# Performance work log

Hardware: AMD Instinct MI355X
Metric: run time of the kernel (lower is better)

The kernel has to match this reference:

```python
import jax, jax.numpy as jnp
import numpy as np

N_NODES = 400
HID = 96
DEC = 64
FEAT_STATIC = 8
FEAT = FEAT_STATIC + N_NODES  # 408
EPS = 1e-8


def prelu(x, a):
    # single-parameter PReLU (torch default num_parameters=1)
    return jnp.where(x >= 0, x, a * x)


def setup_inputs() -> dict:
    key = jax.random.key(0)
    ks = jax.random.split(key, 16)
    B = 16
    E = N_NODES * (N_NODES - 1) // 2  # 79800

    x = jax.random.normal(ks[0], (B, E), dtype=jnp.float32)
    node_features = jax.random.normal(ks[1], (B, N_NODES, FEAT_STATIC), dtype=jnp.float32)
    sc_matrix = jax.random.uniform(ks[2], (B, N_NODES, N_NODES), dtype=jnp.float32)

    # normalization buffers (computed from train split in torch; random stand-ins)
    static_mean = jax.random.normal(ks[3], (1, 1, FEAT_STATIC), dtype=jnp.float32) * 0.1
    static_std = jnp.ones((1, 1, FEAT_STATIC), dtype=jnp.float32)

    def lin(k, fin, fout):
        kw, kb = jax.random.split(k)
        lim = 1.0 / np.sqrt(fin)
        W = jax.random.uniform(kw, (fin, fout), minval=-lim, maxval=lim, dtype=jnp.float32)
        b = jax.random.uniform(kb, (fout,), minval=-lim, maxval=lim, dtype=jnp.float32)
        return W, b

    W_e1, b_e1 = lin(ks[4], FEAT, HID)
    W_e2, b_e2 = lin(ks[5], HID, HID)
    W_d1, b_d1 = lin(ks[6], 3 * HID, DEC)  # symmetric decoder: 3 * node_embed_dim
    W_d2, b_d2 = lin(ks[7], DEC, DEC)
    W_d3, b_d3 = lin(ks[8], DEC, 1)

    a25 = jnp.float32(0.25)

    ei_np, ej_np = np.triu_indices(N_NODES, k=1)
    ei = jnp.asarray(ei_np, dtype=jnp.int32)
    ej = jnp.asarray(ej_np, dtype=jnp.int32)

    return {
        "x": x, "node_features": node_features, "sc_matrix": sc_matrix,
        "static_mean": static_mean, "static_std": static_std,
        "W_e1": W_e1, "b_e1": b_e1, "a_e1": a25,
        "W_e2": W_e2, "b_e2": b_e2, "a_e2": a25,
        "W_d1": W_d1, "b_d1": b_d1, "a_d1": a25,
        "W_d2": W_d2, "b_d2": b_d2, "a_d2": a25,
        "W_d3": W_d3, "b_d3": b_d3,
        "ei": ei, "ej": ej,
    }


def reference(x, node_features, sc_matrix, static_mean, static_std,
              W_e1, b_e1, a_e1, W_e2, b_e2, a_e2,
              W_d1, b_d1, a_d1, W_d2, b_d2, a_d2, W_d3, b_d3, ei, ej):
    # x (SC upper triangle) is only used for batch size in the torch module.
    # static anatomical block: z-score with train stats
    s = (node_features - static_mean) / (static_std + EPS)  # [B,N,8]
    # sc_row block, 'brain_scale': divide by per-matrix mean
    m = sc_matrix / jnp.maximum(
        jnp.mean(sc_matrix, axis=(-2, -1), keepdims=True), EPS)  # [B,N,N]
    feats = jnp.concatenate([s, m], axis=-1)  # [B,N,408]

    # shared node encoder (dropout inactive at eval)
    h = prelu(feats @ W_e1 + b_e1, a_e1)
    h = prelu(h @ W_e2 + b_e2, a_e2)  # [B,N,96]

    # per-edge gather over upper-triangle indices
    h_i = h[:, ei, :]  # [B,E,96]
    h_j = h[:, ej, :]
    # symmetric edge features
    edge_feat = jnp.concatenate(
        [h_i + h_j, jnp.abs(h_i - h_j), h_i * h_j], axis=-1)  # [B,E,288]

    z = prelu(edge_feat @ W_d1 + b_d1, a_d1)
    z = prelu(z @ W_d2 + b_d2, a_d2)
    out = (z @ W_d3 + b_d3)[..., 0]  # [B,E]
    return out
```

## Files before the change

kernel.cpp:

```cpp
#include <hip/hip_runtime.h>

#define NN 400
#define HID 96
#define EDGES 79800
#define BATCH 16
#define ROWS (BATCH*EDGES)
#define NTILES 4988
#define NBLK 512

typedef _Float16 f16;
typedef f16 f16x2 __attribute__((ext_vector_type(2)));
typedef f16 f16x8 __attribute__((ext_vector_type(8)));
typedef __fp16 fp16x2 __attribute__((ext_vector_type(2)));
typedef float f32x16 __attribute__((ext_vector_type(16)));
typedef unsigned int u32;

union H8 { f16x8 h; u32 u[4]; f16x2 p[4]; fp16x2 q[4]; };
union C2 { f16x2 h; fp16x2 q; u32 u; };

__device__ inline f16x2 pkrtz(float a, float b) {
  C2 c; c.q = __builtin_amdgcn_cvt_pkrtz(a, b); return c.h;
}
__device__ inline u32 pkrtz_u(float a, float b) {
  C2 c; c.q = __builtin_amdgcn_cvt_pkrtz(a, b); return c.u;
}
__device__ inline float fdot2a(f16x2 a, f16x2 b, float c) {
#if __has_builtin(__builtin_amdgcn_fdot2)
  C2 ca, cb; ca.h = a; cb.h = b;
  return __builtin_amdgcn_fdot2(ca.q, cb.q, c, false);
#else
  return c + (float)a.x*(float)b.x + (float)a.y*(float)b.y;
#endif
}

__device__ inline f16x8 habs8(f16x8 x) {
  H8 t; t.h = x;
  t.u[0] &= 0x7fff7fffu; t.u[1] &= 0x7fff7fffu;
  t.u[2] &= 0x7fff7fffu; t.u[3] &= 0x7fff7fffu;
  return t.h;
}

__device__ inline f16x8 pack8(float a0,float a1,float a2,float a3,
                              float a4,float a5,float a6,float a7){
  H8 u;
  u.p[0] = pkrtz(a0,a1);
  u.p[1] = pkrtz(a2,a3);
  u.p[2] = pkrtz(a4,a5);
  u.p[3] = pkrtz(a6,a7);
  return u.h;
}

__global__ void prep_mean_kernel(const float* __restrict__ We1, const float* __restrict__ We2,
                                 const float* __restrict__ W1, const float* __restrict__ W2,
                                 const float* __restrict__ sc,
                                 u32* __restrict__ wq, float* __restrict__ mpart) {
  if (blockIdx.x >= 140) {
    int p = blockIdx.x - 140;
    int b = p >> 2, part = p & 3;
    const float4* src = (const float4*)(sc + (size_t)b*160000) + part*10000;
    float s = 0.f;
    for (int i = threadIdx.x; i < 10000; i += 256) {
      float4 v = src[i];
      s += (v.x + v.y) + (v.z + v.w);
    }
    __shared__ float red[256];
    red[threadIdx.x] = s; __syncthreads();
    for (int off = 128; off > 0; off >>= 1) {
      if (threadIdx.x < off) red[threadIdx.x] += red[threadIdx.x + off];
      __syncthreads();
    }
    if (threadIdx.x == 0) mpart[p] = red[0];
    return;
  }
  int D = blockIdx.x*256 + threadIdx.x;
  float v0, v1;
  if (D < 9216) {
    int frag = D >> 8;  int t = frag >> 1, q = frag & 1;
    int rem = D & 255;  int lane = rem >> 2, dj = rem & 3;
    int c = lane & 31, h2 = lane >> 5;
    int k = 16*t + 8*h2 + 2*dj;
    int d = 32*q + c;
    v0 = W1[k*64 + d]; v1 = W1[(k+1)*64 + d];
  } else if (D < 11264) {
    int Dl = D - 9216;
    int frag = Dl >> 8; int t2 = frag >> 1, q = frag & 1;
    int rem = Dl & 255; int lane = rem >> 2, dj = rem & 3;
    int c = lane & 31, h2 = lane >> 5;
    int p = 8*t2 + 4*h2 + dj;
    int d = 32*q + c;
    v0 = W2[p*64 + d]; v1 = W2[(p+32)*64 + d];
  } else if (D < 31232) {
    int Dl = D - 11264;
    int frag = Dl >> 8; int t = frag/3, ct = frag - 3*t;
    int rem = Dl & 255; int lane = rem >> 2, dj = rem & 3;
    int c = lane & 31, h2 = lane >> 5;
    int k0 = 16*t + 8*h2 + 2*dj, k1 = k0 + 1;
    int d = 32*ct + c;
    v0 = (k0 < 400) ? We1[(8+k0)*96 + d] : (k0 < 408 ? We1[(k0-400)*96 + d] : 0.f);
    v1 = (k1 < 400) ? We1[(8+k1)*96 + d] : (k1 < 408 ? We1[(k1-400)*96 + d] : 0.f);
  } else {
    int Dl = D - 31232;
    int frag = Dl >> 8; int t = frag/3, ct = frag - 3*t;
    int rem = Dl & 255; int lane = rem >> 2, dj = rem & 3;
    int c = lane & 31, h2 = lane >> 5;
    int k = 16*t + 8*h2 + 2*dj;
    int d = 32*ct + c;
    v0 = We2[k*96 + d]; v1 = We2[(k+1)*96 + d];
  }
  wq[D] = pkrtz_u(v0, v1);
}

__global__ __launch_bounds__(64) void enc1_kernel(
    const float* __restrict__ sc, const float* __restrict__ nf,
    const float* __restrict__ smean, const float* __restrict__ sstd,
    const float* __restrict__ be1, const float* __restrict__ ae1,
    const float* __restrict__ mpart, const u32* __restrict__ wq,
    f16* __restrict__ g1) {
  int lane = threadIdx.x;
  int rt = blockIdx.x;
  int c = lane & 31, h2 = lane >> 5;
  int r = rt*32 + c;
  int b = r / 400;
  float ms = mpart[4*b] + mpart[4*b+1] + mpart[4*b+2] + mpart[4*b+3];
  float rm = 1.f / fmaxf(ms*(1.f/160000.f), 1e-8f);
  float a = *ae1;
  f32x16 acc[3];
#pragma unroll
  for (int q = 0; q < 3; ++q) {
    float bv = be1[32*q + c];
#pragma unroll
    for (int i = 0; i < 16; ++i) acc[q][i] = bv;
  }
  const u32* wb = wq + 11264;
  const float* scr = sc + (size_t)r*400;
#pragma unroll 4
  for (int t = 0; t < 25; ++t) {
    int k0 = 16*t + 8*h2;
    float4 s0 = *(const float4*)(scr + k0);
    float4 s1 = *(const float4*)(scr + k0 + 4);
    f16x8 af = pack8(s0.x*rm, s0.y*rm, s0.z*rm, s0.w*rm,
                     s1.x*rm, s1.y*rm, s1.z*rm, s1.w*rm);
#pragma unroll
    for (int ct = 0; ct < 3; ++ct) {
      f16x8 bf = *(const f16x8*)(wb + ((t*3+ct)*64 + lane)*4);
      acc[ct] = __builtin_amdgcn_mfma_f32_32x32x16_f16(af, bf, acc[ct], 0,0,0);
    }
  }
  {
    f16x8 af = {};
    if (h2 == 0) {
      float q0[8];
#pragma unroll
      for (int j = 0; j < 8; ++j)
        q0[j] = (nf[r*8 + j] - smean[j]) / (sstd[j] + 1e-8f);
      af = pack8(q0[0],q0[1],q0[2],q0[3],q0[4],q0[5],q0[6],q0[7]);
    }
#pragma unroll
    for (int ct = 0; ct < 3; ++ct) {
      f16x8 bf = *(const f16x8*)(wb + ((25*3+ct)*64 + lane)*4);
      acc[ct] = __builtin_amdgcn_mfma_f32_32x32x16_f16(af, bf, acc[ct], 0,0,0);
    }
  }
#pragma unroll
  for (int ct = 0; ct < 3; ++ct)
#pragma unroll
    for (int rr = 0; rr < 16; ++rr) {
      int row = (rr & 3) + 8*(rr >> 2) + 4*h2;
      float v = acc[ct][rr]; v = fmaxf(v, a*v);
      g1[(rt*32 + row)*96 + 32*ct + c] = (f16)v;
    }
}

__global__ __launch_bounds__(64) void enc2_kernel(
    const f16* __restrict__ g1, const float* __restrict__ be2,
    const float* __restrict__ ae2, const u32* __restrict__ wq,
    f16* __restrict__ hout) {
  int lane = threadIdx.x;
  int rt = blockIdx.x;
  int c = lane & 31, h2 = lane >> 5;
  int r = rt*32 + c;
  float a = *ae2;
  f32x16 acc[3];
#pragma unroll
  for (int q = 0; q < 3; ++q) {
    float bv = be2[32*q + c];
#pragma unroll
    for (int i = 0; i < 16; ++i) acc[q][i] = bv;
  }
  const u32* wb = wq + 31232;
#pragma unroll
  for (int t = 0; t < 6; ++t) {
    f16x8 af = *(const f16x8*)(g1 + r*96 + 16*t + 8*h2);
#pragma unroll
    for (int ct = 0; ct < 3; ++ct) {
      f16x8 bf = *(const f16x8*)(wb + ((t*3+ct)*64 + lane)*4);
      acc[ct] = __builtin_amdgcn_mfma_f32_32x32x16_f16(af, bf, acc[ct], 0,0,0);
    }
  }
#pragma unroll
  for (int ct = 0; ct < 3; ++ct)
#pragma unroll
    for (int rr = 0; rr < 16; ++rr) {
      int row = (rr & 3) + 8*(rr >> 2) + 4*h2;
      float v = acc[ct][rr]; v = fmaxf(v, a*v);
      hout[(rt*32 + row)*96 + 32*ct + c] = (f16)v;
    }
}

__global__ __launch_bounds__(256, 2) void decoder_kernel(
    const f16* __restrict__ hbuf, const u32* __restrict__ wq,
    const float* __restrict__ b1, const float* __restrict__ b2,
    const float* __restrict__ ad1, const float* __restrict__ ad2,
    const float* __restrict__ W3, const float* __restrict__ b3p,
    const int* __restrict__ ei, const int* __restrict__ ej,
    float* __restrict__ out) {
  __shared__ f16 wfr[17408];
  __shared__ u32 zbuf[4][1152];
  {
    float4* dst = (float4*)wfr;
    const float4* src = (const float4*)wq;
    for (int i = threadIdx.x; i < 2176; i += 256) dst[i] = src[i];
  }
  __syncthreads();
  const int lane = threadIdx.x & 63;
  const int wid  = threadIdx.x >> 6;
  const int c = lane & 31, h2 = lane >> 5;
  u32* zb = zbuf[wid];
  f16x8 bp5[2];
  bp5[0] = *(const f16x8*)(wq + ((34+0)*64 + lane)*4);
  bp5[1] = *(const f16x8*)(wq + ((34+1)*64 + lane)*4);
  f16x8 w2f[4][2];
#pragma unroll
  for (int t2 = 0; t2 < 4; ++t2) {
    w2f[t2][0] = *(const f16x8*)(wq + 9216 + ((t2*2+0)*64 + lane)*4);
    w2f[t2][1] = *(const f16x8*)(wq + 9216 + ((t2*2+1)*64 + lane)*4);
  }
  const float b1x = b1[c], b1y = b1[c+32];
  const float b2x = b2[c], b2y = b2[c+32];
  const float a1 = *ad1, a2 = *ad2, b3 = *b3p;
  const f16x2 a1v = pkrtz(a1, a1);
  const f16x2 a2v = pkrtz(a2, a2);
  const f16x2 w3p = pkrtz(W3[c], W3[c+32]);
  const f16x2 ones2 = pkrtz(1.f, 1.f);

  for (int tile = blockIdx.x; tile < NTILES; tile += NBLK) {
    const int rbase = tile*256 + wid*64;
    const f16* pi[2]; const f16* pj[2];
    bool valid[2];
#pragma unroll
    for (int m = 0; m < 2; ++m) {
      int r = rbase + 32*m + c;
      valid[m] = (r < ROWS);
      unsigned rr = valid[m] ? (unsigned)r : (unsigned)(ROWS-1);
      unsigned bb = rr / (unsigned)EDGES;
      int e = (int)(rr - bb*(unsigned)EDGES);
      int ii = ei[e], jj = ej[e];
      pi[m] = hbuf + (((int)bb*NN + ii)*HID + 8*h2);
      pj[m] = hbuf + (((int)bb*NN + jj)*HID + 8*h2);
    }
    f32x16 acc[2][2];
#pragma unroll
    for (int r = 0; r < 16; ++r) {
      acc[0][0][r] = b1x; acc[0][1][r] = b1y;
      acc[1][0][r] = b1x; acc[1][1][r] = b1y;
    }
#pragma unroll
    for (int t = 0; t < 6; ++t) {
      f16x8 bs0 = *(const f16x8*)(wfr + (((t   )*2+0)*64 + lane)*8);
      f16x8 bs1 = *(const f16x8*)(wfr + (((t   )*2+1)*64 + lane)*8);
      f16x8 bd0 = *(const f16x8*)(wfr + (((t+ 6)*2+0)*64 + lane)*8);
      f16x8 bd1 = *(const f16x8*)(wfr + (((t+ 6)*2+1)*64 + lane)*8);
      f16x8 bp0 = (t < 5) ? *(const f16x8*)(wfr + (((t+12)*2+0)*64 + lane)*8) : bp5[0];
      f16x8 bp1 = (t < 5) ? *(const f16x8*)(wfr + (((t+12)*2+1)*64 + lane)*8) : bp5[1];
#pragma unroll
      for (int m = 0; m < 2; ++m) {
        f16x8 hi = *(const f16x8*)(pi[m] + 16*t);
        f16x8 hj = *(const f16x8*)(pj[m] + 16*t);
        f16x8 su = hi + hj;
        f16x8 di = habs8(hi - hj);
        f16x8 pr = hi * hj;
        acc[m][0] = __builtin_amdgcn_mfma_f32_32x32x16_f16(su, bs0, acc[m][0], 0,0,0);
        acc[m][1] = __builtin_amdgcn_mfma_f32_32x32x16_f16(su, bs1, acc[m][1], 0,0,0);
        acc[m][0] = __builtin_amdgcn_mfma_f32_32x32x16_f16(di, bd0, acc[m][0], 0,0,0);
        acc[m][1] = __builtin_amdgcn_mfma_f32_32x32x16_f16(di, bd1, acc[m][1], 0,0,0);
        acc[m][0] = __builtin_amdgcn_mfma_f32_32x32x16_f16(pr, bp0, acc[m][0], 0,0,0);
        acc[m][1] = __builtin_amdgcn_mfma_f32_32x32x16_f16(pr, bp1, acc[m][1], 0,0,0);
      }
    }
#pragma unroll
    for (int m = 0; m < 2; ++m) {
#pragma unroll
      for (int r = 0; r < 16; ++r) {
        f16x2 p = pkrtz(acc[m][0][r], acc[m][1][r]);
        p = __builtin_elementwise_max(p, p * a1v);
        C2 cv; cv.h = p;
        int row = (r & 3) + 8*(r >> 2) + 4*h2;
        zb[row*36 + c] = cv.u;
      }
      f16x8 za[4];
#pragma unroll
      for (int t2 = 0; t2 < 4; ++t2)
        za[t2] = *(const f16x8*)((const f16*)zb + (c*36 + 8*t2 + 4*h2)*2);
      f32x16 zacc[2];
#pragma unroll
      for (int r = 0; r < 16; ++r) { zacc[0][r] = b2x; zacc[1][r] = b2y; }
#pragma unroll
      for (int t2 = 0; t2 < 4; ++t2) {
        zacc[0] = __builtin_amdgcn_mfma_f32_32x32x16_f16(za[t2], w2f[t2][0], zacc[0], 0,0,0);
        zacc[1] = __builtin_amdgcn_mfma_f32_32x32x16_f16(za[t2], w2f[t2][1], zacc[1], 0,0,0);
      }
#pragma unroll
      for (int r = 0; r < 16; ++r) {
        f16x2 p = pkrtz(zacc[0][r], zacc[1][r]);
        p = __builtin_elementwise_max(p, p * a2v);
        p = p * w3p;
        C2 cv; cv.h = p;
        int row = (r & 3) + 8*(r >> 2) + 4*h2;
        zb[row*36 + c] = cv.u;
      }
      float ssum = 0.f;
#pragma unroll
      for (int g = 0; g < 4; ++g) {
        H8 v; v.h = *(const f16x8*)((const f16*)zb + (c*36 + 16*h2 + 4*g)*2);
#pragma unroll
        for (int dw = 0; dw < 4; ++dw)
          ssum = fdot2a(v.p[dw], ones2, ssum);
      }
      ssum += __shfl_xor(ssum, 32);
      if (h2 == 0 && valid[m]) out[rbase + 32*m + c] = ssum + b3;
    }
  }
}

extern "C" void kernel_launch(void* const* d_in, const int* in_sizes, int n_in,
                              void* d_out, int out_size, void* d_ws, size_t ws_size,
                              hipStream_t stream) {
  const float* nf  = (const float*)d_in[1];
  const float* sc  = (const float*)d_in[2];
  const float* sm  = (const float*)d_in[3];
  const float* ss  = (const float*)d_in[4];
  const float* We1 = (const float*)d_in[5];
  const float* be1 = (const float*)d_in[6];
  const float* ae1 = (const float*)d_in[7];
  const float* We2 = (const float*)d_in[8];
  const float* be2 = (const float*)d_in[9];
  const float* ae2 = (const float*)d_in[10];
  const float* W1  = (const float*)d_in[11];
  const float* b1  = (const float*)d_in[12];
  const float* a1  = (const float*)d_in[13];
  const float* W2  = (const float*)d_in[14];
  const float* b2  = (const float*)d_in[15];
  const float* a2  = (const float*)d_in[16];
  const float* W3  = (const float*)d_in[17];
  const float* b3  = (const float*)d_in[18];
  const int*   ei  = (const int*)d_in[19];
  const int*   ej  = (const int*)d_in[20];
  float* out = (float*)d_out;

  char* ws = (char*)d_ws;
  float* mpart = (float*)ws;
  f16*   g1   = (f16*)(ws + 256);
  f16*   hbuf = (f16*)(ws + 256 + 1228800);
  u32*   wq   = (u32*)(ws + 256 + 2*1228800);

  prep_mean_kernel<<<204, 256, 0, stream>>>(We1, We2, W1, W2, sc, wq, mpart);
  enc1_kernel<<<200, 64, 0, stream>>>(sc, nf, sm, ss, be1, ae1, mpart, wq, g1);
  enc2_kernel<<<200, 64, 0, stream>>>(g1, be2, ae2, wq, hbuf);
  decoder_kernel<<<NBLK, 256, 0, stream>>>(hbuf, wq, b1, b2, a1, a2, W3, b3,
                                           ei, ej, out);
}
```

Measured before the change: 193.7 us.

## Fuse encoder layers via LDS staging, prefetch edge indices, raise decoder grid

Measured after the change: 208.4 us. 7.6% more time.

```diff
diff --git a/kernel.cpp b/kernel.cpp
--- a/kernel.cpp
+++ b/kernel.cpp
@@ -6,7 +6,7 @@
 #define BATCH 16
 #define ROWS (BATCH*EDGES)
 #define NTILES 4988
-#define NBLK 512
+#define NBLK 768
 
 typedef _Float16 f16;
 typedef f16 f16x2 __attribute__((ext_vector_type(2)));
@@ -14,8 +14,9 @@
 typedef __fp16 fp16x2 __attribute__((ext_vector_type(2)));
 typedef float f32x16 __attribute__((ext_vector_type(16)));
 typedef unsigned int u32;
-
-union H8 { f16x8 h; u32 u[4]; f16x2 p[4]; fp16x2 q[4]; };
+typedef unsigned long long u64;
+
+union H8 { f16x8 h; u32 u[4]; f16x2 p[4]; fp16x2 q[4]; u64 d[2]; };
 union C2 { f16x2 h; fp16x2 q; u32 u; };
 
 __device__ inline f16x2 pkrtz(float a, float b) {
@@ -104,26 +105,45 @@
     int rem = Dl & 255; int lane = rem >> 2, dj = rem & 3;
     int c = lane & 31, h2 = lane >> 5;
     int k = 16*t + 8*h2 + 2*dj;
+    int p0 = (k   < 64) ? ((k&1)*32 + (k>>1))       : k;
+    int p1 = (k+1 < 64) ? (((k+1)&1)*32 + ((k+1)>>1)) : (k+1);
     int d = 32*ct + c;
-    v0 = We2[k*96 + d]; v1 = We2[(k+1)*96 + d];
+    v0 = We2[p0*96 + d]; v1 = We2[p1*96 + d];
   }
   wq[D] = pkrtz_u(v0, v1);
 }
 
-__global__ __launch_bounds__(64) void enc1_kernel(
+#define EST 210
+__global__ __launch_bounds__(64) void enc_kernel(
     const float* __restrict__ sc, const float* __restrict__ nf,
     const float* __restrict__ smean, const float* __restrict__ sstd,
     const float* __restrict__ be1, const float* __restrict__ ae1,
+    const float* __restrict__ be2, const float* __restrict__ ae2,
     const float* __restrict__ mpart, const u32* __restrict__ wq,
-    f16* __restrict__ g1) {
-  int lane = threadIdx.x;
-  int rt = blockIdx.x;
-  int c = lane & 31, h2 = lane >> 5;
-  int r = rt*32 + c;
-  int b = r / 400;
-  float ms = mpart[4*b] + mpart[4*b+1] + mpart[4*b+2] + mpart[4*b+3];
-  float rm = 1.f / fmaxf(ms*(1.f/160000.f), 1e-8f);
-  float a = *ae1;
+    f16* __restrict__ hout) {
+  __shared__ u32 st[32*EST];
+  const int lane = threadIdx.x;
+  const int rt = blockIdx.x;
+  const int r0 = rt*32;
+  {
+    int row = lane >> 1, half = lane & 1;
+    int r = r0 + row;
+    int b = r / 400;
+    float ms = mpart[4*b] + mpart[4*b+1] + mpart[4*b+2] + mpart[4*b+3];
+    float rm = 1.f / fmaxf(ms*(1.f/160000.f), 1e-8f);
+    const float4* src = (const float4*)(sc + (size_t)r*400) + half*50;
+    u32* dst = st + row*EST + half*100;
+#pragma unroll 5
+    for (int i = 0; i < 50; ++i) {
+      float4 v = src[i];
+      u32 lo = pkrtz_u(v.x*rm, v.y*rm);
+      u32 hi = pkrtz_u(v.z*rm, v.w*rm);
+      u64 w = (u64)lo | ((u64)hi << 32);
+      *(u64*)(dst + 2*i) = w;
+    }
+  }
+  const int c = lane & 31, h2 = lane >> 5;
+  const float a1 = *ae1, a2 = *ae2;
   f32x16 acc[3];
 #pragma unroll
   for (int q = 0; q < 3; ++q) {
@@ -131,24 +151,23 @@
 #pragma unroll
     for (int i = 0; i < 16; ++i) acc[q][i] = bv;
   }
-  const u32* wb = wq + 11264;
-  const float* scr = sc + (size_t)r*400;
-#pragma unroll 4
+  const u32* wb1 = wq + 11264;
+#pragma unroll 5
   for (int t = 0; t < 25; ++t) {
-    int k0 = 16*t + 8*h2;
-    float4 s0 = *(const float4*)(scr + k0);
-    float4 s1 = *(const float4*)(scr + k0 + 4);
-    f16x8 af = pack8(s0.x*rm, s0.y*rm, s0.z*rm, s0.w*rm,
-                     s1.x*rm, s1.y*rm, s1.z*rm, s1.w*rm);
+    H8 av;
+    const u32* ap = st + c*EST + 8*t + 4*h2;
+    av.d[0] = *(const u64*)ap;
+    av.d[1] = *(const u64*)(ap + 2);
 #pragma unroll
     for (int ct = 0; ct < 3; ++ct) {
-      f16x8 bf = *(const f16x8*)(wb + ((t*3+ct)*64 + lane)*4);
-      acc[ct] = __builtin_amdgcn_mfma_f32_32x32x16_f16(af, bf, acc[ct], 0,0,0);
+      f16x8 bf = *(const f16x8*)(wb1 + ((t*3+ct)*64 + lane)*4);
+      acc[ct] = __builtin_amdgcn_mfma_f32_32x32x16_f16(av.h, bf, acc[ct], 0,0,0);
     }
   }
   {
     f16x8 af = {};
     if (h2 == 0) {
+      int r = r0 + c;
       float q0[8];
 #pragma unroll
       for (int j = 0; j < 8; ++j)
@@ -157,8 +176,35 @@
     }
 #pragma unroll
     for (int ct = 0; ct < 3; ++ct) {
-      f16x8 bf = *(const f16x8*)(wb + ((25*3+ct)*64 + lane)*4);
+      f16x8 bf = *(const f16x8*)(wb1 + ((25*3+ct)*64 + lane)*4);
       acc[ct] = __builtin_amdgcn_mfma_f32_32x32x16_f16(af, bf, acc[ct], 0,0,0);
+    }
+  }
+  u32* zb = st;
+#pragma unroll
+  for (int r = 0; r < 16; ++r) {
+    float x0 = acc[0][r]; x0 = fmaxf(x0, a1*x0);
+    float x1 = acc[1][r]; x1 = fmaxf(x1, a1*x1);
+    float x2 = acc[2][r]; x2 = fmaxf(x2, a1*x2);
+    int row = (r & 3) + 8*(r >> 2) + 4*h2;
+    zb[row*52 + c] = pkrtz_u(x0, x1);
+    ((f16*)zb)[row*104 + 64 + c] = (f16)x2;
+  }
+  f32x16 acc2[3];
+#pragma unroll
+  for (int q = 0; q < 3; ++q) {
+    float bv = be2[32*q + c];
+#pragma unroll
+    for (int i = 0; i < 16; ++i) acc2[q][i] = bv;
+  }
+  const u32* wb2 = wq + 31232;
+#pragma unroll
+  for (int t = 0; t < 6; ++t) {
+    f16x8 af = *(const f16x8*)((const f16*)zb + c*104 + 16*t + 8*h2);
+#pragma unroll
+    for (int ct = 0; ct < 3; ++ct) {
+      f16x8 bf = *(const f16x8*)(wb2 + ((t*3+ct)*64 + lane)*4);
+      acc2[ct] = __builtin_amdgcn_mfma_f32_32x32x16_f16(af, bf, acc2[ct], 0,0,0);
     }
   }
 #pragma unroll
@@ -166,44 +212,8 @@
 #pragma unroll
     for (int rr = 0; rr < 16; ++rr) {
       int row = (rr & 3) + 8*(rr >> 2) + 4*h2;
-      float v = acc[ct][rr]; v = fmaxf(v, a*v);
-      g1[(rt*32 + row)*96 + 32*ct + c] = (f16)v;
-    }
-}
-
-__global__ __launch_bounds__(64) void enc2_kernel(
-    const f16* __restrict__ g1, const float* __restrict__ be2,
-    const float* __restrict__ ae2, const u32* __restrict__ wq,
-    f16* __restrict__ hout) {
-  int lane = threadIdx.x;
-  int rt = blockIdx.x;
-  int c = lane & 31, h2 = lane >> 5;
-  int r = rt*32 + c;
-  float a = *ae2;
-  f32x16 acc[3];
-#pragma unroll
-  for (int q = 0; q < 3; ++q) {
-    float bv = be2[32*q + c];
-#pragma unroll
-    for (int i = 0; i < 16; ++i) acc[q][i] = bv;
-  }
-  const u32* wb = wq + 31232;
-#pragma unroll
-  for (int t = 0; t < 6; ++t) {
-    f16x8 af = *(const f16x8*)(g1 + r*96 + 16*t + 8*h2);
-#pragma unroll
-    for (int ct = 0; ct < 3; ++ct) {
-      f16x8 bf = *(const f16x8*)(wb + ((t*3+ct)*64 + lane)*4);
-      acc[ct] = __builtin_amdgcn_mfma_f32_32x32x16_f16(af, bf, acc[ct], 0,0,0);
-    }
-  }
-#pragma unroll
-  for (int ct = 0; ct < 3; ++ct)
-#pragma unroll
-    for (int rr = 0; rr < 16; ++rr) {
-      int row = (rr & 3) + 8*(rr >> 2) + 4*h2;
-      float v = acc[ct][rr]; v = fmaxf(v, a*v);
-      hout[(rt*32 + row)*96 + 32*ct + c] = (f16)v;
+      float v = acc2[ct][rr]; v = fmaxf(v, a2*v);
+      hout[(r0 + row)*96 + 32*ct + c] = (f16)v;
     }
 }
 
@@ -243,20 +253,41 @@
   const f16x2 w3p = pkrtz(W3[c], W3[c+32]);
   const f16x2 ones2 = pkrtz(1.f, 1.f);
 
-  for (int tile = blockIdx.x; tile < NTILES; tile += NBLK) {
+  int tile = blockIdx.x;
+  int nii[2], njj[2]; bool nvalid[2];
+#pragma unroll
+  for (int m = 0; m < 2; ++m) {
+    int r = tile*256 + wid*64 + 32*m + c;
+    nvalid[m] = (r < ROWS);
+    unsigned rr = nvalid[m] ? (unsigned)r : (unsigned)(ROWS-1);
+    unsigned bb = rr / (unsigned)EDGES;
+    int e = (int)(rr - bb*(unsigned)EDGES);
+    nii[m] = (int)(bb*NN) + ei[e];
+    njj[m] = (int)(bb*NN) + ej[e];
+  }
+
+  for (; tile < NTILES; tile += NBLK) {
     const int rbase = tile*256 + wid*64;
     const f16* pi[2]; const f16* pj[2];
     bool valid[2];
 #pragma unroll
     for (int m = 0; m < 2; ++m) {
-      int r = rbase + 32*m + c;
-      valid[m] = (r < ROWS);
-      unsigned rr = valid[m] ? (unsigned)r : (unsigned)(ROWS-1);
-      unsigned bb = rr / (unsigned)EDGES;
-      int e = (int)(rr - bb*(unsigned)EDGES);
-      int ii = ei[e], jj = ej[e];
-      pi[m] = hbuf + (((int)bb*NN + ii)*HID + 8*h2);
-      pj[m] = hbuf + (((int)bb*NN + jj)*HID + 8*h2);
+      valid[m] = nvalid[m];
+      pi[m] = hbuf + (nii[m]*HID + 8*h2);
+      pj[m] = hbuf + (njj[m]*HID + 8*h2);
+    }
+    int ntile = tile + NBLK;
+    if (ntile < NTILES) {
+#pragma unroll
+      for (int m = 0; m < 2; ++m) {
+        int r = ntile*256 + wid*64 + 32*m + c;
+        nvalid[m] = (r < ROWS);
+        unsigned rr = nvalid[m] ? (unsigned)r : (unsigned)(ROWS-1);
+        unsigned bb = rr / (unsigned)EDGES;
+        int e = (int)(rr - bb*(unsigned)EDGES);
+        nii[m] = (int)(bb*NN) + ei[e];
+        njj[m] = (int)(bb*NN) + ej[e];
+      }
     }
     f32x16 acc[2][2];
 #pragma unroll
@@ -359,13 +390,12 @@
 
   char* ws = (char*)d_ws;
   float* mpart = (float*)ws;
-  f16*   g1   = (f16*)(ws + 256);
-  f16*   hbuf = (f16*)(ws + 256 + 1228800);
-  u32*   wq   = (u32*)(ws + 256 + 2*1228800);
+  f16*   hbuf = (f16*)(ws + 256);
+  u32*   wq   = (u32*)(ws + 256 + 1228800);
 
   prep_mean_kernel<<<204, 256, 0, stream>>>(We1, We2, W1, W2, sc, wq, mpart);
-  enc1_kernel<<<200, 64, 0, stream>>>(sc, nf, sm, ss, be1, ae1, mpart, wq, g1);
-  enc2_kernel<<<200, 64, 0, stream>>>(g1, be2, ae2, wq, hbuf);
+  enc_kernel<<<200, 64, 0, stream>>>(sc, nf, sm, ss, be1, ae1, be2, ae2,
+                                     mpart, wq, hbuf);
   decoder_kernel<<<NBLK, 256, 0, stream>>>(hbuf, wq, b1, b2, a1, a2, W3, b3,
                                            ei, ej, out);
 }
```
